# Performance work log

Hardware: AMD Instinct MI355X
Metric: run time of the kernel (lower is better)

## Reference

```python
import jax, jax.numpy as jnp
import numpy as np

B, C, D, H, W = 16, 8, 511, 16, 16
NHEADS = 16
DIM = C * H * W          # 2048 hidden size
SEQ = D + 1              # 512 tokens incl. cls
HEAD_DIM = DIM // NHEADS # 128


def setup_inputs() -> dict:
    key = jax.random.key(0)
    ks = jax.random.split(key, 8)
    s = 0.02  # weight init scale
    return {
        "x": jax.random.normal(ks[0], (B, C, D, H, W), jnp.float32),
        "pos_embedding": jax.random.normal(ks[1], (1, SEQ, DIM), jnp.float32),
        "cls": jax.random.normal(ks[2], (1, 1, DIM), jnp.float32),
        "qkv_w": jax.random.normal(ks[3], (DIM, 3 * DIM), jnp.float32) * s,
        "qkv_b": jnp.zeros((3 * DIM,), jnp.float32),
        "proj_w": jax.random.normal(ks[4], (DIM, DIM), jnp.float32) * s,
        "proj_b": jnp.zeros((DIM,), jnp.float32),
    }


def reference(x, pos_embedding, cls, qkv_w, qkv_b, proj_w, proj_b):
    b = x.shape[0]
    # rearrange 'b c d h w -> b d (c h w)'
    tok = jnp.transpose(x, (0, 2, 1, 3, 4)).reshape(b, D, DIM)
    tok = jnp.concatenate([jnp.broadcast_to(cls, (b, 1, DIM)), tok], axis=1)
    tok = tok + pos_embedding  # (b, SEQ, DIM)
    # qkv projection (dropout probs are 0 -> identity)
    qkv = tok @ qkv_w + qkv_b  # (b, SEQ, 3*DIM)
    qkv = qkv.reshape(b, SEQ, 3, NHEADS, HEAD_DIM).transpose(2, 0, 3, 1, 4)
    q, k, v = qkv[0], qkv[1], qkv[2]  # each (b, nH, SEQ, hd)
    scale = HEAD_DIM ** -0.5
    score = jax.nn.softmax(jnp.einsum('bhqd,bhkd->bhqk', q, k) * scale, axis=-1)
    out = jnp.einsum('bhqk,bhkd->bhqd', score, v)
    out = out.transpose(0, 2, 1, 3).reshape(b, SEQ, DIM)
    out = out @ proj_w + proj_b
    return out[:, 0]  # cls token, (b, DIM)
```

## Files before the change

### kernel.cpp

```cpp
#include <hip/hip_runtime.h>


#define BB   16
#define CC   8
#define DD   511
#define DIM  2048
#define SEQ  512
#define NH   16
#define HD   128
#define W3   6144
#define SCALE 0.08838834764831845f

#define Q_OFF   0
#define AO_OFF  2048
#define R_OFF   34816
#define G_OFF   67584
#define SC_OFF  67600
#define U_OFF   198672
#define RB_OFF  722960

typedef __attribute__((ext_vector_type(8))) short short8;
typedef __attribute__((ext_vector_type(4))) float floatx4;

static __device__ inline short bf_hi(float f) {
  return (short)(__float_as_uint(f) >> 16);
}
static __device__ inline float bf_hif(float f) {
  return __uint_as_float(__float_as_uint(f) & 0xffff0000u);
}

__global__ __launch_bounds__(256) void k1_q(
    const float* __restrict__ pos, const float* __restrict__ cls,
    const float* __restrict__ qkv_w, const float* __restrict__ qkv_b,
    float* __restrict__ ws) {
  int n  = blockIdx.x * 256 + threadIdx.x;
  int d0 = blockIdx.y * 32;
  float acc = (blockIdx.y == 0) ? qkv_b[n] : 0.f;
#pragma unroll 8
  for (int d = d0; d < d0 + 32; ++d) {
    float t0 = cls[d] + pos[d];
    acc += t0 * qkv_w[(size_t)d * W3 + n];
  }
  atomicAdd(&ws[Q_OFF + n], acc);
}

__global__ __launch_bounds__(128) void k2_r(
    const float* __restrict__ qkv_w, float* __restrict__ ws) {
  __shared__ float qs[HD];
  int h = blockIdx.y;
  int d = blockIdx.x * 128 + threadIdx.x;
  if (threadIdx.x < HD) qs[threadIdx.x] = ws[Q_OFF + h * HD + threadIdx.x];
  __syncthreads();
  const float4* w4 = reinterpret_cast<const float4*>(
      qkv_w + (size_t)d * W3 + DIM + h * HD);
  float acc = 0.f;
#pragma unroll 8
  for (int e4 = 0; e4 < 32; ++e4) {
    float4 w = w4[e4];
    acc += qs[e4*4+0]*w.x + qs[e4*4+1]*w.y + qs[e4*4+2]*w.z + qs[e4*4+3]*w.w;
  }
  float r = acc * SCALE;
  int i = h * DIM + d;
  ws[R_OFF + i] = r;
  short* rb = (short*)(ws + RB_OFF);
  short hi = bf_hi(r);
  rb[i] = hi;
  rb[NH * DIM + i] = bf_hi(r - bf_hif(r));
}

__global__ __launch_bounds__(256) void k2b_gamma(
    const float* __restrict__ pos, const float* __restrict__ cls,
    float* __restrict__ ws) {
  __shared__ float red[256];
  int h = blockIdx.x, t = threadIdx.x;
  float part = 0.f;
  for (int d = t; d < DIM; d += 256)
    part += (cls[d] + pos[d]) * ws[R_OFF + h * DIM + d];
  red[t] = part;
  __syncthreads();
  for (int s = 128; s > 0; s >>= 1) {
    if (t < s) red[t] += red[t + s];
    __syncthreads();
  }
  if (t == 0) ws[G_OFF + h] = red[0];
}

__global__ __launch_bounds__(64) void k3_scores_mfma(
    const float* __restrict__ x, const float* __restrict__ pos,
    float* __restrict__ ws) {
  int jt = blockIdx.x, b = blockIdx.y, ks = blockIdx.z;
  int l  = threadIdx.x;
  int m  = l & 15;
  int kg = l >> 4;
  int jrow = 1 + jt * 16 + m;
  int jc = jrow < SEQ ? jrow : (SEQ - 1);
  const size_t xrow = (size_t)b * CC * DD * 256 + (size_t)(jc - 1) * 256;
  const short* rh = (const short*)(ws + RB_OFF);
  const short* rl = rh + NH * DIM;
  floatx4 acc = {0.f, 0.f, 0.f, 0.f};
#pragma unroll 2
  for (int kk = ks * 16; kk < ks * 16 + 16; ++kk) {
    int d0 = kk * 32 + kg * 8;
    int c = d0 >> 8, doff = d0 & 255;
    const float4* xp = reinterpret_cast<const float4*>(
        x + xrow + (size_t)c * DD * 256 + doff);
    const float4* pp = reinterpret_cast<const float4*>(
        pos + (size_t)jc * DIM + d0);
    float4 xa = xp[0], xb = xp[1];
    float4 pa = pp[0], pb = pp[1];
    float f[8] = {xa.x + pa.x, xa.y + pa.y, xa.z + pa.z, xa.w + pa.w,
                  xb.x + pb.x, xb.y + pb.y, xb.z + pb.z, xb.w + pb.w};
    short8 ahi, alo;
#pragma unroll
    for (int i = 0; i < 8; ++i) {
      ahi[i] = bf_hi(f[i]);
      alo[i] = bf_hi(f[i] - bf_hif(f[i]));
    }
    short8 bhi = *reinterpret_cast<const short8*>(rh + m * DIM + d0);
    short8 blo = *reinterpret_cast<const short8*>(rl + m * DIM + d0);
    acc = __builtin_amdgcn_mfma_f32_16x16x32_bf16(ahi, bhi, acc, 0, 0, 0);
    acc = __builtin_amdgcn_mfma_f32_16x16x32_bf16(ahi, blo, acc, 0, 0, 0);
    acc = __builtin_amdgcn_mfma_f32_16x16x32_bf16(alo, bhi, acc, 0, 0, 0);
  }
  int h = m;
#pragma unroll
  for (int reg = 0; reg < 4; ++reg) {
    int row = kg * 4 + reg;
    int j = 1 + jt * 16 + row;
    if (j < SEQ)
      atomicAdd(&ws[SC_OFF + (size_t)(b * NH + h) * SEQ + j], acc[reg]);
  }
}

__global__ __launch_bounds__(256) void k4_softmax(float* __restrict__ ws) {
  int h = blockIdx.x, b = blockIdx.y, t = threadIdx.x;
  float* sc = ws + SC_OFF + (size_t)(b * NH + h) * SEQ;
  __shared__ float red[256];
  float s0 = (t == 0) ? ws[G_OFF + h] : sc[t];
  float s1 = sc[t + 256];
  red[t] = fmaxf(s0, s1);
  __syncthreads();
  for (int s = 128; s > 0; s >>= 1) { if (t < s) red[t] = fmaxf(red[t], red[t + s]); __syncthreads(); }
  float m = red[0];
  __syncthreads();
  float e0 = __expf(s0 - m), e1 = __expf(s1 - m);
  red[t] = e0 + e1;
  __syncthreads();
  for (int s = 128; s > 0; s >>= 1) { if (t < s) red[t] += red[t + s]; __syncthreads(); }
  float inv = 1.f / red[0];
  sc[t] = e0 * inv;
  sc[t + 256] = e1 * inv;
}

__global__ __launch_bounds__(256) void k5_u(
    const float* __restrict__ x, const float* __restrict__ pos,
    const float* __restrict__ cls, float* __restrict__ ws) {
  int c = blockIdx.x, qc = blockIdx.y, b = blockIdx.z, t = threadIdx.x;
  int d = c * 256 + t;
  __shared__ float pl[NH][64];
  __shared__ float pl0[NH];
  const float* pp = ws + SC_OFF + (size_t)b * NH * SEQ;
  int j0 = 1 + qc * 64;
  for (int i = t; i < NH * 64; i += 256) {
    int h = i >> 6, jj = i & 63;
    int j = j0 + jj;
    pl[h][jj] = (j < SEQ) ? pp[h * SEQ + j] : 0.f;
  }
  if (t < NH) pl0[t] = pp[t * SEQ];
  __syncthreads();
  float acc[NH];
  if (qc == 0) {
    float t0 = cls[d] + pos[d];
#pragma unroll
    for (int h = 0; h < NH; ++h) acc[h] = pl0[h] * t0;
  } else {
#pragma unroll
    for (int h = 0; h < NH; ++h) acc[h] = 0.f;
  }
  const size_t xb = (size_t)b * CC * DD * 256 + (size_t)c * DD * 256 + t;
  const float* posc = pos + c * 256 + t;
#pragma unroll 2
  for (int jt = 0; jt < 64; jt += 4) {
    float xvv[4];
#pragma unroll
    for (int jj = 0; jj < 4; ++jj) {
      int j = j0 + jt + jj;
      xvv[jj] = (j < SEQ)
          ? x[xb + (size_t)(j - 1) * 256] + posc[(size_t)j * DIM]
          : 0.f;
    }
#pragma unroll
    for (int h = 0; h < NH; ++h) {
      float4 p4 = *reinterpret_cast<const float4*>(&pl[h][jt]);
      acc[h] += p4.x * xvv[0] + p4.y * xvv[1] + p4.z * xvv[2] + p4.w * xvv[3];
    }
  }
  float* u = ws + U_OFF + (size_t)(b * NH) * DIM + d;
#pragma unroll
  for (int h = 0; h < NH; ++h) atomicAdd(&u[(size_t)h * DIM], acc[h]);
}

__global__ __launch_bounds__(256) void k6_ao(
    const float* __restrict__ qkv_w, const float* __restrict__ qkv_b,
    float* __restrict__ ws) {
  int nt = blockIdx.x, dc = blockIdx.y, t = threadIdx.x;
  int m = nt * 256 + t;
  int h0 = nt * 2;
  int d0 = dc * 32;
  __shared__ float us[2][32][20];
  for (int i = t; i < 2 * 32 * BB; i += 256) {
    int dd = i & 31, b = (i >> 5) & 15, hh = i >> 9;
    us[hh][dd][b] = ws[U_OFF + (size_t)(b * NH + h0 + hh) * DIM + d0 + dd];
  }
  __syncthreads();
  int hl = t >> 7;
  float acc[BB];
#pragma unroll
  for (int b = 0; b < BB; ++b) acc[b] = 0.f;
  const float* wcol = qkv_w + (size_t)d0 * W3 + 2 * DIM + m;
#pragma unroll 4
  for (int dd = 0; dd < 32; ++dd) {
    float w = wcol[(size_t)dd * W3];
    const float4* u4 = reinterpret_cast<const float4*>(&us[hl][dd][0]);
    float4 u0 = u4[0], u1 = u4[1], u2 = u4[2], u3 = u4[3];
    acc[0]  += u0.x * w; acc[1]  += u0.y * w; acc[2]  += u0.z * w; acc[3]  += u0.w * w;
    acc[4]  += u1.x * w; acc[5]  += u1.y * w; acc[6]  += u1.z * w; acc[7]  += u1.w * w;
    acc[8]  += u2.x * w; acc[9]  += u2.y * w; acc[10] += u2.z * w; acc[11] += u2.w * w;
    acc[12] += u3.x * w; acc[13] += u3.y * w; acc[14] += u3.z * w; acc[15] += u3.w * w;
  }
  float bias = (dc == 0) ? qkv_b[2 * DIM + m] : 0.f;
#pragma unroll
  for (int b = 0; b < BB; ++b)
    atomicAdd(&ws[AO_OFF + b * DIM + m], acc[b] + bias);
}

__global__ __launch_bounds__(256) void k7_out(
    const float* __restrict__ proj_w, const float* __restrict__ proj_b,
    const float* __restrict__ ws, float* __restrict__ out) {
  int nt = blockIdx.x, mc = blockIdx.y, t = threadIdx.x;
  int n = nt * 256 + t;
  int m0 = mc * 32;
  __shared__ float as[32][20];
  for (int i = t; i < 32 * BB; i += 256) {
    int mm = i & 31, b = i >> 5;
    as[mm][b] = ws[AO_OFF + b * DIM + m0 + mm];
  }
  __syncthreads();
  float acc[BB];
#pragma unroll
  for (int b = 0; b < BB; ++b) acc[b] = 0.f;
  const float* wcol = proj_w + (size_t)m0 * DIM + n;
#pragma unroll 4
  for (int mm = 0; mm < 32; ++mm) {
    float w = wcol[(size_t)mm * DIM];
    const float4* a4 = reinterpret_cast<const float4*>(&as[mm][0]);
    float4 a0 = a4[0], a1 = a4[1], a2 = a4[2], a3 = a4[3];
    acc[0]  += a0.x * w; acc[1]  += a0.y * w; acc[2]  += a0.z * w; acc[3]  += a0.w * w;
    acc[4]  += a1.x * w; acc[5]  += a1.y * w; acc[6]  += a1.z * w; acc[7]  += a1.w * w;
    acc[8]  += a2.x * w; acc[9]  += a2.y * w; acc[10] += a2.z * w; acc[11] += a2.w * w;
    acc[12] += a3.x * w; acc[13] += a3.y * w; acc[14] += a3.z * w; acc[15] += a3.w * w;
  }
  float bias = (mc == 0) ? proj_b[n] : 0.f;
#pragma unroll
  for (int b = 0; b < BB; ++b)
    atomicAdd(&out[b * DIM + n], acc[b] + bias);
}

extern "C" void kernel_launch(void* const* d_in, const int* in_sizes, int n_in,
                              void* d_out, int out_size, void* d_ws, size_t ws_size,
                              hipStream_t stream) {
  const float* x      = (const float*)d_in[0];
  const float* pos    = (const float*)d_in[1];
  const float* cls    = (const float*)d_in[2];
  const float* qkv_w  = (const float*)d_in[3];
  const float* qkv_b  = (const float*)d_in[4];
  const float* proj_w = (const float*)d_in[5];
  const float* proj_b = (const float*)d_in[6];
  float* ws  = (float*)d_ws;
  float* out = (float*)d_out;

  hipMemsetAsync(ws, 0, (size_t)RB_OFF * sizeof(float), stream);
  hipMemsetAsync(out, 0, (size_t)out_size * sizeof(float), stream);

  k1_q          <<<dim3(8, 64),     256, 0, stream>>>(pos, cls, qkv_w, qkv_b, ws);
  k2_r          <<<dim3(16, 16),    128, 0, stream>>>(qkv_w, ws);
  k2b_gamma     <<<16,              256, 0, stream>>>(pos, cls, ws);
  k3_scores_mfma<<<dim3(32, 16, 4),  64, 0, stream>>>(x, pos, ws);
  k4_softmax    <<<dim3(16, 16),    256, 0, stream>>>(ws);
  k5_u          <<<dim3(8, 8, 16),  256, 0, stream>>>(x, pos, cls, ws);
  k6_ao         <<<dim3(8, 64),     256, 0, stream>>>(qkv_w, qkv_b, ws);
  k7_out        <<<dim3(8, 64),     256, 0, stream>>>(proj_w, proj_b, ws, out);
}
```

Baseline: 248.9 us.

## Use split-bf16 MFMA for probability-weighted token sum and fuse gamma into k2

Replaces the scalar FP32 P·(x+pos) accumulation kernel with an MFMA kernel. It stages probabilities as hi/lo bf16 pairs in shared memory and uses three bf16 MFMAs per tile to approximate FP32 accuracy. The kernel writes U directly, without atomics, so the U region no longer needs zeroing and the workspace layout is reordered to shrink the memset. The gamma reduction is folded into k2_r through a wave shuffle and an atomic add, which removes one launch. The split-bf16 scheme carries some accuracy risk, and the grid is smaller (512 blocks).

```diff
diff --git a/kernel.cpp b/kernel.cpp
--- a/kernel.cpp
+++ b/kernel.cpp
@@ -13,11 +13,12 @@
 
 #define Q_OFF   0
 #define AO_OFF  2048
-#define R_OFF   34816
-#define G_OFF   67584
-#define SC_OFF  67600
-#define U_OFF   198672
-#define RB_OFF  722960
+#define G_OFF   34816
+#define SC_OFF  34832
+#define ZERO_N  165904
+#define R_OFF   165904
+#define RB_OFF  198672
+#define U_OFF   231440
 
 typedef __attribute__((ext_vector_type(8))) short short8;
 typedef __attribute__((ext_vector_type(4))) float floatx4;
@@ -45,7 +46,8 @@
 }
 
 __global__ __launch_bounds__(128) void k2_r(
-    const float* __restrict__ qkv_w, float* __restrict__ ws) {
+    const float* __restrict__ qkv_w, const float* __restrict__ pos,
+    const float* __restrict__ cls, float* __restrict__ ws) {
   __shared__ float qs[HD];
   int h = blockIdx.y;
   int d = blockIdx.x * 128 + threadIdx.x;
@@ -63,26 +65,11 @@
   int i = h * DIM + d;
   ws[R_OFF + i] = r;
   short* rb = (short*)(ws + RB_OFF);
-  short hi = bf_hi(r);
-  rb[i] = hi;
+  rb[i] = bf_hi(r);
   rb[NH * DIM + i] = bf_hi(r - bf_hif(r));
-}
-
-__global__ __launch_bounds__(256) void k2b_gamma(
-    const float* __restrict__ pos, const float* __restrict__ cls,
-    float* __restrict__ ws) {
-  __shared__ float red[256];
-  int h = blockIdx.x, t = threadIdx.x;
-  float part = 0.f;
-  for (int d = t; d < DIM; d += 256)
-    part += (cls[d] + pos[d]) * ws[R_OFF + h * DIM + d];
-  red[t] = part;
-  __syncthreads();
-  for (int s = 128; s > 0; s >>= 1) {
-    if (t < s) red[t] += red[t + s];
-    __syncthreads();
-  }
-  if (t == 0) ws[G_OFF + h] = red[0];
+  float g = (cls[d] + pos[d]) * r;
+  for (int m = 1; m < 64; m <<= 1) g += __shfl_xor(g, m, 64);
+  if ((threadIdx.x & 63) == 0) atomicAdd(&ws[G_OFF + h], g);
 }
 
 __global__ __launch_bounds__(64) void k3_scores_mfma(
@@ -152,52 +139,59 @@
   sc[t + 256] = e1 * inv;
 }
 
-__global__ __launch_bounds__(256) void k5_u(
+#define PSTR 520
+__global__ __launch_bounds__(256) void k5_pv_mfma(
     const float* __restrict__ x, const float* __restrict__ pos,
     const float* __restrict__ cls, float* __restrict__ ws) {
-  int c = blockIdx.x, qc = blockIdx.y, b = blockIdx.z, t = threadIdx.x;
-  int d = c * 256 + t;
-  __shared__ float pl[NH][64];
-  __shared__ float pl0[NH];
-  const float* pp = ws + SC_OFF + (size_t)b * NH * SEQ;
-  int j0 = 1 + qc * 64;
-  for (int i = t; i < NH * 64; i += 256) {
-    int h = i >> 6, jj = i & 63;
-    int j = j0 + jj;
-    pl[h][jj] = (j < SEQ) ? pp[h * SEQ + j] : 0.f;
-  }
-  if (t < NH) pl0[t] = pp[t * SEQ];
-  __syncthreads();
-  float acc[NH];
-  if (qc == 0) {
-    float t0 = cls[d] + pos[d];
-#pragma unroll
-    for (int h = 0; h < NH; ++h) acc[h] = pl0[h] * t0;
-  } else {
-#pragma unroll
-    for (int h = 0; h < NH; ++h) acc[h] = 0.f;
-  }
-  const size_t xb = (size_t)b * CC * DD * 256 + (size_t)c * DD * 256 + t;
-  const float* posc = pos + c * 256 + t;
-#pragma unroll 2
-  for (int jt = 0; jt < 64; jt += 4) {
-    float xvv[4];
-#pragma unroll
-    for (int jj = 0; jj < 4; ++jj) {
-      int j = j0 + jt + jj;
-      xvv[jj] = (j < SEQ)
-          ? x[xb + (size_t)(j - 1) * 256] + posc[(size_t)j * DIM]
-          : 0.f;
+  int dt = blockIdx.x, b = blockIdx.y, t = threadIdx.x;
+  __shared__ short phl[NH * PSTR];
+  __shared__ short pll[NH * PSTR];
+  const float* pb = ws + SC_OFF + (size_t)b * NH * SEQ;
+  for (int i = t; i < NH * SEQ; i += 256) {
+    int h = i >> 9, j = i & 511;
+    float v = pb[h * SEQ + j];
+    phl[h * PSTR + j] = bf_hi(v);
+    pll[h * PSTR + j] = bf_hi(v - bf_hif(v));
+  }
+  __syncthreads();
+  int w = t >> 6, l = t & 63;
+  int m16 = l & 15, kq = l >> 4;
+  int dcol = dt * 64 + w * 16 + m16;
+  int c = dcol >> 8, doff = dcol & 255;
+  const float* xcol = x + (size_t)b * CC * DD * 256 + (size_t)c * DD * 256 + doff;
+  const float* pcol = pos + dcol;
+  float clsv0 = cls[dcol];
+  const short8* pph = reinterpret_cast<const short8*>(&phl[m16 * PSTR]);
+  const short8* ppl = reinterpret_cast<const short8*>(&pll[m16 * PSTR]);
+  floatx4 acc = {0.f, 0.f, 0.f, 0.f};
+  for (int kk = 0; kk < 16; ++kk) {
+    int jb = kk * 32 + kq * 8;
+    const float* xp = xcol + ((size_t)jb - 1) * 256;
+    const float* xp_safe = (jb == 0) ? xcol : xp;
+    float f[8];
+    float x0 = xp_safe[0];
+    f[0] = ((jb == 0) ? clsv0 : x0) + pcol[(size_t)jb * DIM];
+#pragma unroll
+    for (int e = 1; e < 8; ++e)
+      f[e] = xp[(size_t)e * 256] + pcol[(size_t)(jb + e) * DIM];
+    short8 thi, tlo;
+#pragma unroll
+    for (int i = 0; i < 8; ++i) {
+      thi[i] = bf_hi(f[i]);
+      tlo[i] = bf_hi(f[i] - bf_hif(f[i]));
     }
-#pragma unroll
-    for (int h = 0; h < NH; ++h) {
-      float4 p4 = *reinterpret_cast<const float4*>(&pl[h][jt]);
-      acc[h] += p4.x * xvv[0] + p4.y * xvv[1] + p4.z * xvv[2] + p4.w * xvv[3];
-    }
-  }
-  float* u = ws + U_OFF + (size_t)(b * NH) * DIM + d;
-#pragma unroll
-  for (int h = 0; h < NH; ++h) atomicAdd(&u[(size_t)h * DIM], acc[h]);
+    short8 phi = pph[kk * 4 + kq];
+    short8 plo = ppl[kk * 4 + kq];
+    acc = __builtin_amdgcn_mfma_f32_16x16x32_bf16(phi, thi, acc, 0, 0, 0);
+    acc = __builtin_amdgcn_mfma_f32_16x16x32_bf16(phi, tlo, acc, 0, 0, 0);
+    acc = __builtin_amdgcn_mfma_f32_16x16x32_bf16(plo, thi, acc, 0, 0, 0);
+  }
+  float* ub = ws + U_OFF + (size_t)b * NH * DIM + dcol;
+#pragma unroll
+  for (int reg = 0; reg < 4; ++reg) {
+    int h = kq * 4 + reg;
+    ub[(size_t)h * DIM] = acc[reg];
+  }
 }
 
 __global__ __launch_bounds__(256) void k6_ao(
@@ -279,15 +273,14 @@
   float* ws  = (float*)d_ws;
   float* out = (float*)d_out;
 
-  hipMemsetAsync(ws, 0, (size_t)RB_OFF * sizeof(float), stream);
+  hipMemsetAsync(ws, 0, (size_t)ZERO_N * sizeof(float), stream);
   hipMemsetAsync(out, 0, (size_t)out_size * sizeof(float), stream);
 
   k1_q          <<<dim3(8, 64),     256, 0, stream>>>(pos, cls, qkv_w, qkv_b, ws);
-  k2_r          <<<dim3(16, 16),    128, 0, stream>>>(qkv_w, ws);
-  k2b_gamma     <<<16,              256, 0, stream>>>(pos, cls, ws);
+  k2_r          <<<dim3(16, 16),    128, 0, stream>>>(qkv_w, pos, cls, ws);
   k3_scores_mfma<<<dim3(32, 16, 4),  64, 0, stream>>>(x, pos, ws);
   k4_softmax    <<<dim3(16, 16),    256, 0, stream>>>(ws);
-  k5_u          <<<dim3(8, 8, 16),  256, 0, stream>>>(x, pos, cls, ws);
+  k5_pv_mfma    <<<dim3(32, 16),    256, 0, stream>>>(x, pos, cls, ws);
   k6_ao         <<<dim3(8, 64),     256, 0, stream>>>(qkv_w, qkv_b, ws);
   k7_out        <<<dim3(8, 64),     256, 0, stream>>>(proj_w, proj_b, ws, out);
 }
```

Result: faster. 222.1 us (-10.8%).
